# Performance work log

Hardware: AMD Instinct MI355X
Metric: run time of the kernel (lower is better)

## Reference

```python
import jax, jax.numpy as jnp
import numpy as np

D = 42            # node hidden dim
ED = 10           # edge feature dim
B = 512           # graphs per batch
NU, EU = 16384, 32768   # solute nodes/edges (32 nodes per graph)
NV, EV = 20480, 40960   # solvent nodes/edges (40 nodes per graph)
STEPS = 6


def setup_inputs() -> dict:
    key = jax.random.key(0)
    ks = iter(jax.random.split(key, 48))
    nrm = lambda shape, s: jax.random.normal(next(ks), shape, dtype=jnp.float32) * s
    inp = {}
    inp["su_x"] = nrm((NU, D), 1.0)
    inp["su_e"] = nrm((EU, ED), 1.0)
    inp["su_src"] = jax.random.randint(next(ks), (EU,), 0, NU, dtype=jnp.int32)
    inp["su_dst"] = jax.random.randint(next(ks), (EU,), 0, NU, dtype=jnp.int32)
    inp["sv_x"] = nrm((NV, D), 1.0)
    inp["sv_e"] = nrm((EV, ED), 1.0)
    inp["sv_src"] = jax.random.randint(next(ks), (EV,), 0, NV, dtype=jnp.int32)
    inp["sv_dst"] = jax.random.randint(next(ks), (EV,), 0, NV, dtype=jnp.int32)
    for p in ("su", "sv"):
        inp[p + "_lin0_w"] = nrm((D, D), D ** -0.5)
        inp[p + "_lin0_b"] = jnp.zeros((D,), jnp.float32)
        inp[p + "_msg_w"] = nrm((D, D), D ** -0.5)
        inp[p + "_msg_b"] = jnp.zeros((D,), jnp.float32)
        inp[p + "_en1_w"] = nrm((ED, ED), ED ** -0.5)
        inp[p + "_en1_b"] = jnp.zeros((ED,), jnp.float32)
        inp[p + "_en2_w"] = nrm((ED, D * D), 0.02)  # small scale keeps 6-step recursion stable
        inp[p + "_en2_b"] = jnp.zeros((D * D,), jnp.float32)
        inp[p + "_conv_b"] = jnp.zeros((D,), jnp.float32)
    inp["fc1_w"] = nrm((4 * D, 256), (4 * D) ** -0.5)
    inp["fc1_b"] = jnp.zeros((256,), jnp.float32)
    inp["fc2_w"] = nrm((256, 128), 256 ** -0.5)
    inp["fc2_b"] = jnp.zeros((128,), jnp.float32)
    inp["fc3_w"] = nrm((128, 1), 128 ** -0.5)
    inp["fc3_b"] = jnp.zeros((1,), jnp.float32)
    return inp


def _gather(x, efeat, src, dst, lw, lb, mw, mb, e1w, e1b, e2w, e2b, cb, n_nodes):
    """GatherModel: lin0 + 6 x (NNConv(sum, residual=identity, bias) -> relu -> message_layer -> relu) + skip."""
    init = x
    out = jax.nn.relu(x @ lw + lb)
    # Edge network depends only on static edge features -> compute per-edge 42x42 once.
    We = (jax.nn.relu(efeat @ e1w + e1b) @ e2w + e2b).reshape(-1, D, D)  # [E, D, D]
    for _ in range(STEPS):
        msg = jnp.einsum('ei,eio->eo', out[src], We)                    # gather + per-edge matvec
        agg = jax.ops.segment_sum(msg, dst, num_segments=n_nodes)      # scatter-add
        m = jax.nn.relu(agg + out + cb)                                 # residual (identity) + bias, then relu
        out = jax.nn.relu(m @ mw + mb)
    return out + init


def reference(su_x, su_e, su_src, su_dst, sv_x, sv_e, sv_src, sv_dst,
              su_lin0_w, su_lin0_b, su_msg_w, su_msg_b, su_en1_w, su_en1_b, su_en2_w, su_en2_b, su_conv_b,
              sv_lin0_w, sv_lin0_b, sv_msg_w, sv_msg_b, sv_en1_w, sv_en1_b, sv_en2_w, sv_en2_b, sv_conv_b,
              fc1_w, fc1_b, fc2_w, fc2_b, fc3_w, fc3_b):
    su = _gather(su_x, su_e, su_src, su_dst, su_lin0_w, su_lin0_b, su_msg_w, su_msg_b,
                 su_en1_w, su_en1_b, su_en2_w, su_en2_b, su_conv_b, NU)
    sv = _gather(sv_x, sv_e, sv_src, sv_dst, sv_lin0_w, sv_lin0_b, sv_msg_w, sv_msg_b,
                 sv_en1_w, sv_en1_b, sv_en2_w, sv_en2_b, sv_conv_b, NV)
    # per-graph mean pooling (equal-sized graphs -> reshape)
    su_emb = su.reshape(B, NU // B, D).mean(axis=1)          # [B, D]
    sv_emb = sv.reshape(B, NV // B, D).mean(axis=1)
    su_fin = jnp.concatenate([su_emb, su_emb], axis=1)       # [B, 2D]
    sv_fin = jnp.concatenate([sv_emb, sv_emb], axis=1)
    su_g = su_fin.mean(axis=0, keepdims=True)                # [1, 2D] (code means over batch)
    sv_g = sv_fin.mean(axis=0, keepdims=True)
    comb = jnp.concatenate([su_g, sv_g], axis=1)             # [1, 4D]
    h = jax.nn.relu(comb @ fc1_w + fc1_b)                    # dropout is identity at inference
    h = jax.nn.relu(h @ fc2_w + fc2_b)
    pred = h @ fc3_w + fc3_b                                 # [1, 1]
    interaction = jnp.zeros((su.shape[0], sv.shape[0]), jnp.float32)
    return pred, interaction
```

## Files before the change

### kernel.cpp

```cpp
#include <hip/hip_runtime.h>

#define D   42
#define ED  10
#define NU  16384
#define EU  32768
#define NV  20480
#define EV  40960
#define NT  (NU + NV)
#define ET  (EU + EV)
#define GJ  462
#define GP  464
#define STEPS 6

typedef float floatx4 __attribute__((ext_vector_type(4)));

__global__ void k_prep(const float* __restrict__ su_w2, const float* __restrict__ su_b2,
                       const float* __restrict__ sv_w2, const float* __restrict__ sv_b2,
                       float* __restrict__ A, float* __restrict__ mean) {
    int gid = blockIdx.x * 256 + threadIdx.x;
    if (gid < 128) mean[gid] = 0.f;
    if (gid >= 2 * D * GP) return;
    int phase = gid / (D * GP);
    int r = gid - phase * D * GP;
    int i = r / GP, j = r - i * GP;
    const float* w2 = phase ? sv_w2 : su_w2;
    const float* b2 = phase ? sv_b2 : su_b2;
    float v = 0.f;
    if (j < GJ) {
        int k = j / D, o = j - k * D;
        v = (k < ED) ? w2[k * (D * D) + i * D + o] : b2[i * D + o];
    }
    A[gid] = v;
}

__global__ void k_zcnt(int* __restrict__ p, int n) {
    int gid = blockIdx.x * 256 + threadIdx.x;
    if (gid < n) p[gid] = 0;
}

__global__ void k_count(const int* __restrict__ su_src, const int* __restrict__ su_dst,
                        const int* __restrict__ sv_src, const int* __restrict__ sv_dst,
                        int* __restrict__ outDeg, int* __restrict__ inDeg) {
    int e = blockIdx.x * 256 + threadIdx.x;
    if (e >= ET) return;
    int src, dst;
    if (e < EU) { src = su_src[e];           dst = su_dst[e]; }
    else        { src = sv_src[e - EU] + NU; dst = sv_dst[e - EU] + NU; }
    atomicAdd(&outDeg[src], 1);
    atomicAdd(&inDeg[dst], 1);
}

__global__ __launch_bounds__(1024) void k_scan(const int* __restrict__ degO, int* __restrict__ offO,
                                               const int* __restrict__ degI, int* __restrict__ offI) {
    __shared__ int part[1024];
    int t = threadIdx.x;
    for (int a = 0; a < 2; a++) {
        const int* deg = a ? degI : degO;
        int* off = a ? offI : offO;
        int loc[36];
        int base = t * 36;
        int s = 0;
        #pragma unroll
        for (int j = 0; j < 36; j++) { loc[j] = s; s += deg[base + j]; }
        part[t] = s;
        __syncthreads();
        for (int d = 1; d < 1024; d <<= 1) {
            int v = (t >= d) ? part[t - d] : 0;
            __syncthreads();
            part[t] += v;
            __syncthreads();
        }
        int excl = part[t] - s;
        #pragma unroll
        for (int j = 0; j < 36; j++) off[base + j] = excl + loc[j];
        if (t == 1023) off[NT] = excl + s;
        __syncthreads();
    }
}

__global__ void k_place(const int* __restrict__ su_src, const int* __restrict__ su_dst,
                        const int* __restrict__ sv_src, const int* __restrict__ sv_dst,
                        const int* __restrict__ offO, int* __restrict__ cntO,
                        const int* __restrict__ offI, int* __restrict__ cntI,
                        int* __restrict__ inList, int* __restrict__ srcSorted,
                        int* __restrict__ pOf) {
    int e = blockIdx.x * 256 + threadIdx.x;
    if (e >= ET) return;
    int src, dst;
    if (e < EU) { src = su_src[e];           dst = su_dst[e]; }
    else        { src = sv_src[e - EU] + NU; dst = sv_dst[e - EU] + NU; }
    int p = offO[src] + atomicAdd(&cntO[src], 1);
    int q = offI[dst] + atomicAdd(&cntI[dst], 1);
    inList[q] = p;
    srcSorted[p] = src;
    pOf[e] = p;
}

__global__ void k_edgeh(const float* __restrict__ su_e, const float* __restrict__ sv_e,
                        const float* __restrict__ su_w1, const float* __restrict__ su_b1,
                        const float* __restrict__ sv_w1, const float* __restrict__ sv_b1,
                        const int* __restrict__ pOf, float* __restrict__ hs) {
    __shared__ float w1s[2][ED * ED];
    __shared__ float b1s[2][ED];
    int tid = threadIdx.x;
    if (tid < ED * ED) { w1s[0][tid] = su_w1[tid]; w1s[1][tid] = sv_w1[tid]; }
    if (tid < ED)      { b1s[0][tid] = su_b1[tid]; b1s[1][tid] = sv_b1[tid]; }
    __syncthreads();
    int e = blockIdx.x * 256 + tid;
    if (e >= ET) return;
    int ph = (e >= EU);
    const float* ef = ph ? (sv_e + (size_t)(e - EU) * ED) : (su_e + (size_t)e * ED);
    float v[ED];
    #pragma unroll
    for (int j = 0; j < ED; j++) v[j] = ef[j];
    size_t p = (size_t)pOf[e] * 12;
    #pragma unroll
    for (int k = 0; k < ED; k++) {
        float s = b1s[ph][k];
        #pragma unroll
        for (int j = 0; j < ED; j++) s += v[j] * w1s[ph][j * ED + k];
        hs[p + k] = fmaxf(s, 0.f);
    }
    hs[p + 10] = 1.f;
    hs[p + 11] = 0.f;
}

__global__ __launch_bounds__(512, 1) void k_step(float* __restrict__ out,
                                                 const float* __restrict__ A,
                                                 const int* __restrict__ offO,
                                                 const int* __restrict__ srcSorted,
                                                 const float* __restrict__ hs,
                                                 float* __restrict__ msgW,
                                                 const float* __restrict__ msgR,
                                                 const int* __restrict__ offI,
                                                 const int* __restrict__ inList,
                                                 const float* __restrict__ su_x,
                                                 const float* __restrict__ sv_x,
                                                 const float* __restrict__ su_W, const float* __restrict__ su_b,
                                                 const float* __restrict__ sv_W, const float* __restrict__ sv_b,
                                                 const float* __restrict__ su_cb, const float* __restrict__ sv_cb,
                                                 int first) {
    __shared__ float A_lds[D * GP];
    __shared__ float g_lds[32 * GP];
    __shared__ float outT[D * 36];
    __shared__ float mT[D * 36];
    __shared__ float w_lds[D * 48];
    int tid = threadIdx.x;
    int n0 = blockIdx.x * 32;
    int ph = (n0 >= NU);

    const floatx4* Ag = (const floatx4*)(A + (ph ? D * GP : 0));
    floatx4* Al4 = (floatx4*)A_lds;
    for (int idx = tid; idx < D * GP / 4; idx += 512) Al4[idx] = Ag[idx];

    const float* W = ph ? sv_W : su_W;
    const float* b = ph ? sv_b : su_b;
    for (int idx = tid; idx < D * 48; idx += 512) {
        int i = idx / 48, o = idx - i * 48;
        w_lds[idx] = (o < D) ? W[i * D + o] : 0.f;
    }

    if (first) {
        const float* x = ph ? (sv_x + (size_t)(n0 - NU) * D) : (su_x + (size_t)n0 * D);
        for (int idx = tid; idx < 32 * D; idx += 512) {
            int i = idx % D, nn = idx / D;
            mT[i * 36 + nn] = x[(size_t)nn * D + i];
        }
    } else {
        const float* cb = ph ? sv_cb : su_cb;
        for (int idx = tid; idx < 32 * D; idx += 512) {
            int o = idx % D, nn = idx / D;
            int n = n0 + nn;
            int q0 = offI[n], q1 = offI[n + 1];
            float s = out[(size_t)n * D + o] + cb[o];
            for (int q = q0; q < q1; q++) s += msgR[(size_t)inList[q] * D + o];
            mT[o * 36 + nn] = fmaxf(s, 0.f);
        }
    }
    __syncthreads();

    for (int idx = tid; idx < 32 * D; idx += 512) {
        int o = idx % D, nn = idx / D;
        float s = b[o];
        #pragma unroll
        for (int i = 0; i < D; i++) s += mT[i * 36 + nn] * w_lds[i * 48 + o];
        float v = fmaxf(s, 0.f);
        out[(size_t)(n0 + nn) * D + o] = v;
        outT[o * 36 + nn] = v;
    }
    __syncthreads();

    if (tid < 232) {
        int cg = tid % 58, ng = tid / 58;
        const floatx4* oT4 = (const floatx4*)outT;
        floatx4 acc[8][2];
        #pragma unroll
        for (int r = 0; r < 8; r++) { acc[r][0] = (floatx4)(0.f); acc[r][1] = (floatx4)(0.f); }
        for (int k = 0; k < D; k++) {
            floatx4 a0 = Al4[k * 116 + 2 * cg];
            floatx4 a1 = Al4[k * 116 + 2 * cg + 1];
            floatx4 o0 = oT4[k * 9 + 2 * ng];
            floatx4 o1 = oT4[k * 9 + 2 * ng + 1];
            #pragma unroll
            for (int r = 0; r < 4; r++) {
                acc[r][0]     += a0 * o0[r];
                acc[r][1]     += a1 * o0[r];
                acc[r + 4][0] += a0 * o1[r];
                acc[r + 4][1] += a1 * o1[r];
            }
        }
        floatx4* gl4 = (floatx4*)g_lds;
        #pragma unroll
        for (int r = 0; r < 8; r++) {
            gl4[(8 * ng + r) * 116 + 2 * cg]     = acc[r][0];
            gl4[(8 * ng + r) * 116 + 2 * cg + 1] = acc[r][1];
        }
    }
    __syncthreads();

    int p0 = offO[n0], p1 = offO[n0 + 32];
    int nwork = (p1 - p0) * D;
    for (int idx = tid; idx < nwork; idx += 512) {
        int pr = idx / D, o = idx - pr * D;
        int p = p0 + pr;
        int local = srcSorted[p] - n0;
        const float* hrow = hs + (size_t)p * 12;
        const float* grow = g_lds + local * GP;
        float s = 0.f;
        #pragma unroll
        for (int k = 0; k <= ED; k++) s += hrow[k] * grow[k * D + o];
        msgW[(size_t)p * D + o] = s;
    }
}

__global__ __launch_bounds__(256) void k_updF(const int* __restrict__ offI,
                                              const int* __restrict__ inList,
                                              const float* __restrict__ msg,
                                              float* __restrict__ out,
                                              const float* __restrict__ su_mw, const float* __restrict__ su_mb,
                                              const float* __restrict__ su_cb,
                                              const float* __restrict__ sv_mw, const float* __restrict__ sv_mb,
                                              const float* __restrict__ sv_cb) {
    __shared__ float mw_lds[D * D];
    __shared__ float mloc[32 * 44];
    int tid = threadIdx.x;
    int n0 = blockIdx.x * 32;
    int ph = (n0 >= NU);
    const float* mw = ph ? sv_mw : su_mw;
    const float* mb = ph ? sv_mb : su_mb;
    const float* cb = ph ? sv_cb : su_cb;
    for (int idx = tid; idx < D * D; idx += 256) mw_lds[idx] = mw[idx];
    for (int idx = tid; idx < 32 * D; idx += 256) {
        int o = idx % D, nn = idx / D;
        int n = n0 + nn;
        int q0 = offI[n], q1 = offI[n + 1];
        float s = out[(size_t)n * D + o] + cb[o];
        for (int q = q0; q < q1; q++) s += msg[(size_t)inList[q] * D + o];
        mloc[nn * 44 + o] = fmaxf(s, 0.f);
    }
    __syncthreads();
    for (int idx = tid; idx < 32 * D; idx += 256) {
        int o = idx % D, nn = idx / D;
        float s = mb[o];
        #pragma unroll
        for (int i = 0; i < D; i++) s += mloc[nn * 44 + i] * mw_lds[i * D + o];
        out[(size_t)(n0 + nn) * D + o] = fmaxf(s, 0.f);
    }
}

__global__ void k_reduce(const float* __restrict__ out, const float* __restrict__ su_x,
                         const float* __restrict__ sv_x, float* __restrict__ mean) {
    __shared__ float sdata[6 * D];
    int tid = threadIdx.x;
    int bid = blockIdx.x;
    int n0, ph, nl0;
    const float* x;
    if (bid < NU / 128) { ph = 0; n0 = bid * 128;                 nl0 = n0;      x = su_x; }
    else                { ph = 1; n0 = NU + (bid - NU/128) * 128; nl0 = n0 - NU; x = sv_x; }
    if (tid < 6 * D) {
        int o = tid % D, r = tid / D;
        float acc = 0.f;
        for (int nn = r; nn < 128; nn += 6)
            acc += out[(size_t)(n0 + nn) * D + o] + x[(size_t)(nl0 + nn) * D + o];
        sdata[r * D + o] = acc;
    }
    __syncthreads();
    if (tid < D) {
        float tot = 0.f;
        #pragma unroll
        for (int r = 0; r < 6; r++) tot += sdata[r * D + tid];
        atomicAdd(&mean[ph * D + tid], tot);
    }
}

__global__ void k_mlp(const float* __restrict__ mean,
                      const float* __restrict__ fc1w, const float* __restrict__ fc1b,
                      const float* __restrict__ fc2w, const float* __restrict__ fc2b,
                      const float* __restrict__ fc3w, const float* __restrict__ fc3b,
                      float* __restrict__ outp) {
    __shared__ float c[4 * D];
    __shared__ float h1[256];
    __shared__ float h2[128];
    int t = threadIdx.x;
    if (t < 4 * D) {
        float v;
        if (t < 2 * D) v = mean[t < D ? t : t - D] * (1.f / NU);
        else { int q = t - 2 * D; v = mean[D + (q < D ? q : q - D)] * (1.f / NV); }
        c[t] = v;
    }
    __syncthreads();
    float s = fc1b[t];
    for (int j = 0; j < 4 * D; j++) s += c[j] * fc1w[j * 256 + t];
    h1[t] = fmaxf(s, 0.f);
    __syncthreads();
    if (t < 128) {
        float s2 = fc2b[t];
        for (int j = 0; j < 256; j++) s2 += h1[j] * fc2w[j * 128 + t];
        h2[t] = fmaxf(s2, 0.f);
    }
    __syncthreads();
    if (t == 0) {
        float s3 = fc3b[0];
        for (int j = 0; j < 128; j++) s3 += h2[j] * fc3w[j];
        outp[0] = s3;
    }
}

extern "C" void kernel_launch(void* const* d_in, const int* in_sizes, int n_in,
                              void* d_out, int out_size, void* d_ws, size_t ws_size,
                              hipStream_t stream) {
    const float* su_x     = (const float*)d_in[0];
    const float* su_e     = (const float*)d_in[1];
    const int*   su_src   = (const int*)d_in[2];
    const int*   su_dst   = (const int*)d_in[3];
    const float* sv_x     = (const float*)d_in[4];
    const float* sv_e     = (const float*)d_in[5];
    const int*   sv_src   = (const int*)d_in[6];
    const int*   sv_dst   = (const int*)d_in[7];
    const float* su_lin0w = (const float*)d_in[8];
    const float* su_lin0b = (const float*)d_in[9];
    const float* su_msgw  = (const float*)d_in[10];
    const float* su_msgb  = (const float*)d_in[11];
    const float* su_en1w  = (const float*)d_in[12];
    const float* su_en1b  = (const float*)d_in[13];
    const float* su_en2w  = (const float*)d_in[14];
    const float* su_en2b  = (const float*)d_in[15];
    const float* su_convb = (const float*)d_in[16];
    const float* sv_lin0w = (const float*)d_in[17];
    const float* sv_lin0b = (const float*)d_in[18];
    const float* sv_msgw  = (const float*)d_in[19];
    const float* sv_msgb  = (const float*)d_in[20];
    const float* sv_en1w  = (const float*)d_in[21];
    const float* sv_en1b  = (const float*)d_in[22];
    const float* sv_en2w  = (const float*)d_in[23];
    const float* sv_en2b  = (const float*)d_in[24];
    const float* sv_convb = (const float*)d_in[25];
    const float* fc1w     = (const float*)d_in[26];
    const float* fc1b     = (const float*)d_in[27];
    const float* fc2w     = (const float*)d_in[28];
    const float* fc2b     = (const float*)d_in[29];
    const float* fc3w     = (const float*)d_in[30];
    const float* fc3b     = (const float*)d_in[31];

    float* ws   = (float*)d_ws;
    float* out  = ws;
    float* msg0 = out  + (size_t)NT * D;
    float* msg1 = msg0 + (size_t)ET * D;
    float* hs   = msg1 + (size_t)ET * D;
    float* A    = hs   + (size_t)ET * 12;
    float* mean = A    + (size_t)2 * D * GP;
    int* ib     = (int*)(mean + 128);
    int* outDeg = ib;
    int* inDeg  = outDeg + NT;
    int* outCnt = inDeg  + NT;
    int* inCnt  = outCnt + NT;
    int* outOff = inCnt  + NT;
    int* inOff  = outOff + (NT + 1);
    int* inList = inOff  + (NT + 1);
    int* srcS   = inList + ET;
    int* pOf    = srcS   + ET;

    hipMemsetAsync(d_out, 0, (size_t)out_size * sizeof(float), stream);

    k_prep<<<(2 * D * GP + 255) / 256, 256, 0, stream>>>(su_en2w, su_en2b, sv_en2w, sv_en2b, A, mean);

    k_zcnt<<<(4 * NT + 255) / 256, 256, 0, stream>>>(outDeg, 4 * NT);
    k_count<<<(ET + 255) / 256, 256, 0, stream>>>(su_src, su_dst, sv_src, sv_dst, outDeg, inDeg);
    k_scan<<<1, 1024, 0, stream>>>(outDeg, outOff, inDeg, inOff);
    k_place<<<(ET + 255) / 256, 256, 0, stream>>>(su_src, su_dst, sv_src, sv_dst,
                                                  outOff, outCnt, inOff, inCnt, inList, srcS, pOf);
    k_edgeh<<<(ET + 255) / 256, 256, 0, stream>>>(su_e, sv_e, su_en1w, su_en1b, sv_en1w, sv_en1b, pOf, hs);

    float* mbuf[2] = { msg0, msg1 };
    for (int s = 0; s < STEPS; s++) {
        float* mw_ = mbuf[s & 1];
        float* mr_ = mbuf[(s & 1) ^ 1];
        if (s == 0) {
            k_step<<<NT / 32, 512, 0, stream>>>(out, A, outOff, srcS, hs, mw_, nullptr,
                                                inOff, inList, su_x, sv_x,
                                                su_lin0w, su_lin0b, sv_lin0w, sv_lin0b,
                                                su_convb, sv_convb, 1);
        } else {
            k_step<<<NT / 32, 512, 0, stream>>>(out, A, outOff, srcS, hs, mw_, mr_,
                                                inOff, inList, su_x, sv_x,
                                                su_msgw, su_msgb, sv_msgw, sv_msgb,
                                                su_convb, sv_convb, 0);
        }
    }
    k_updF<<<NT / 32, 256, 0, stream>>>(inOff, inList, mbuf[(STEPS - 1) & 1], out,
                                        su_msgw, su_msgb, su_convb, sv_msgw, sv_msgb, sv_convb);

    k_reduce<<<NU / 128 + NV / 128, 256, 0, stream>>>(out, su_x, sv_x, mean);
    k_mlp<<<1, 256, 0, stream>>>(mean, fc1w, fc1b, fc2w, fc2b, fc3w, fc3b, (float*)d_out);
}
```

Measured before the change: 846.9 us.

## Stream edge-net tensor from global and register-tile the small node GEMMs

Drops the per-block LDS copy of the large A matrix in k_step, so the outer-product loop now reads A straight from global/L2 and less LDS is needed. The launch bound is raised to 2 blocks per CU. The 32x42x42 node matmuls in k_step and k_updF are rewritten as register-tiled float4 outer products over 44 threads, with zero-padded mT and weight layouts. This trades LDS footprint and per-block load time for more global traffic on A, and uses only 44 active threads for the small GEMM phase.

```diff
diff --git a/kernel.cpp b/kernel.cpp
--- a/kernel.cpp
+++ b/kernel.cpp
@@ -125,7 +125,7 @@
     hs[p + 11] = 0.f;
 }
 
-__global__ __launch_bounds__(512, 1) void k_step(float* __restrict__ out,
+__global__ __launch_bounds__(512, 2) void k_step(float* __restrict__ out,
                                                  const float* __restrict__ A,
                                                  const int* __restrict__ offO,
                                                  const int* __restrict__ srcSorted,
@@ -140,18 +140,13 @@
                                                  const float* __restrict__ sv_W, const float* __restrict__ sv_b,
                                                  const float* __restrict__ su_cb, const float* __restrict__ sv_cb,
                                                  int first) {
-    __shared__ float A_lds[D * GP];
     __shared__ float g_lds[32 * GP];
     __shared__ float outT[D * 36];
-    __shared__ float mT[D * 36];
+    __shared__ float mT[48 * 36];
     __shared__ float w_lds[D * 48];
     int tid = threadIdx.x;
     int n0 = blockIdx.x * 32;
     int ph = (n0 >= NU);
-
-    const floatx4* Ag = (const floatx4*)(A + (ph ? D * GP : 0));
-    floatx4* Al4 = (floatx4*)A_lds;
-    for (int idx = tid; idx < D * GP / 4; idx += 512) Al4[idx] = Ag[idx];
 
     const float* W = ph ? sv_W : su_W;
     const float* b = ph ? sv_b : su_b;
@@ -159,6 +154,7 @@
         int i = idx / 48, o = idx - i * 48;
         w_lds[idx] = (o < D) ? W[i * D + o] : 0.f;
     }
+    for (int idx = tid; idx < 6 * 36; idx += 512) mT[D * 36 + idx] = 0.f;
 
     if (first) {
         const float* x = ph ? (sv_x + (size_t)(n0 - NU) * D) : (su_x + (size_t)n0 * D);
@@ -179,26 +175,49 @@
     }
     __syncthreads();
 
-    for (int idx = tid; idx < 32 * D; idx += 512) {
-        int o = idx % D, nn = idx / D;
-        float s = b[o];
-        #pragma unroll
-        for (int i = 0; i < D; i++) s += mT[i * 36 + nn] * w_lds[i * 48 + o];
-        float v = fmaxf(s, 0.f);
-        out[(size_t)(n0 + nn) * D + o] = v;
-        outT[o * 36 + nn] = v;
+    if (tid < 44) {
+        int cg = tid % 11, ng = tid / 11;
+        const floatx4* mT4 = (const floatx4*)mT;
+        const floatx4* w4  = (const floatx4*)w_lds;
+        floatx4 accn[8];
+        #pragma unroll
+        for (int r = 0; r < 8; r++) accn[r] = (floatx4)(0.f);
+        for (int k = 0; k < D; k++) {
+            floatx4 m0 = mT4[k * 9 + 2 * ng];
+            floatx4 m1 = mT4[k * 9 + 2 * ng + 1];
+            floatx4 wv = w4[k * 12 + cg];
+            #pragma unroll
+            for (int r = 0; r < 4; r++) {
+                accn[r]     += wv * m0[r];
+                accn[r + 4] += wv * m1[r];
+            }
+        }
+        #pragma unroll
+        for (int r = 0; r < 8; r++) {
+            int nn = 8 * ng + r;
+            #pragma unroll
+            for (int c = 0; c < 4; c++) {
+                int o = 4 * cg + c;
+                if (o < D) {
+                    float v = fmaxf(accn[r][c] + b[o], 0.f);
+                    out[(size_t)(n0 + nn) * D + o] = v;
+                    outT[o * 36 + nn] = v;
+                }
+            }
+        }
     }
     __syncthreads();
 
     if (tid < 232) {
         int cg = tid % 58, ng = tid / 58;
+        const floatx4* Ag = (const floatx4*)(A + (ph ? D * GP : 0));
         const floatx4* oT4 = (const floatx4*)outT;
         floatx4 acc[8][2];
         #pragma unroll
         for (int r = 0; r < 8; r++) { acc[r][0] = (floatx4)(0.f); acc[r][1] = (floatx4)(0.f); }
         for (int k = 0; k < D; k++) {
-            floatx4 a0 = Al4[k * 116 + 2 * cg];
-            floatx4 a1 = Al4[k * 116 + 2 * cg + 1];
+            floatx4 a0 = Ag[k * 116 + 2 * cg];
+            floatx4 a1 = Ag[k * 116 + 2 * cg + 1];
             floatx4 o0 = oT4[k * 9 + 2 * ng];
             floatx4 o1 = oT4[k * 9 + 2 * ng + 1];
             #pragma unroll
@@ -241,30 +260,54 @@
                                               const float* __restrict__ su_cb,
                                               const float* __restrict__ sv_mw, const float* __restrict__ sv_mb,
                                               const float* __restrict__ sv_cb) {
-    __shared__ float mw_lds[D * D];
-    __shared__ float mloc[32 * 44];
+    __shared__ float mT[48 * 36];
+    __shared__ float w_lds[D * 48];
     int tid = threadIdx.x;
     int n0 = blockIdx.x * 32;
     int ph = (n0 >= NU);
     const float* mw = ph ? sv_mw : su_mw;
     const float* mb = ph ? sv_mb : su_mb;
     const float* cb = ph ? sv_cb : su_cb;
-    for (int idx = tid; idx < D * D; idx += 256) mw_lds[idx] = mw[idx];
+    for (int idx = tid; idx < D * 48; idx += 256) {
+        int i = idx / 48, o = idx - i * 48;
+        w_lds[idx] = (o < D) ? mw[i * D + o] : 0.f;
+    }
+    for (int idx = tid; idx < 6 * 36; idx += 256) mT[D * 36 + idx] = 0.f;
     for (int idx = tid; idx < 32 * D; idx += 256) {
         int o = idx % D, nn = idx / D;
         int n = n0 + nn;
         int q0 = offI[n], q1 = offI[n + 1];
         float s = out[(size_t)n * D + o] + cb[o];
         for (int q = q0; q < q1; q++) s += msg[(size_t)inList[q] * D + o];
-        mloc[nn * 44 + o] = fmaxf(s, 0.f);
-    }
-    __syncthreads();
-    for (int idx = tid; idx < 32 * D; idx += 256) {
-        int o = idx % D, nn = idx / D;
-        float s = mb[o];
-        #pragma unroll
-        for (int i = 0; i < D; i++) s += mloc[nn * 44 + i] * mw_lds[i * D + o];
-        out[(size_t)(n0 + nn) * D + o] = fmaxf(s, 0.f);
+        mT[o * 36 + nn] = fmaxf(s, 0.f);
+    }
+    __syncthreads();
+    if (tid < 44) {
+        int cg = tid % 11, ng = tid / 11;
+        const floatx4* mT4 = (const floatx4*)mT;
+        const floatx4* w4  = (const floatx4*)w_lds;
+        floatx4 accn[8];
+        #pragma unroll
+        for (int r = 0; r < 8; r++) accn[r] = (floatx4)(0.f);
+        for (int k = 0; k < D; k++) {
+            floatx4 m0 = mT4[k * 9 + 2 * ng];
+            floatx4 m1 = mT4[k * 9 + 2 * ng + 1];
+            floatx4 wv = w4[k * 12 + cg];
+            #pragma unroll
+            for (int r = 0; r < 4; r++) {
+                accn[r]     += wv * m0[r];
+                accn[r + 4] += wv * m1[r];
+            }
+        }
+        #pragma unroll
+        for (int r = 0; r < 8; r++) {
+            int nn = 8 * ng + r;
+            #pragma unroll
+            for (int c = 0; c < 4; c++) {
+                int o = 4 * cg + c;
+                if (o < D) out[(size_t)(n0 + nn) * D + o] = fmaxf(accn[r][c] + mb[o], 0.f);
+            }
+        }
     }
 }
 
```

After: 2.218 ms. 162% more time.
